# Performance work log

Hardware: AMD Instinct MI355X
Metric: run time of the kernel (lower is better)

The kernel has to match this reference:

```python
import jax, jax.numpy as jnp
import numpy as np

B, L, K, NR, S = 512, 1024, 8, 512, 20  # batch, seq_len, n_matrices, n_rates, alphabet
EXT = 26  # extended alphabet (20 std aa + 6 special), pad of 6 in call()


def _expm(A):
    """Differentiable matrix exponential for small batched matrices (..., n, n).
    Scaling-and-squaring with an order-16 Taylor series (fixed 6 squarings).
    Matches tf.linalg.expm to high accuracy for the small-norm tau*Q here."""
    SQ = 6
    A = A / jnp.asarray(2.0 ** SQ, A.dtype)
    n = A.shape[-1]
    I = jnp.eye(n, dtype=A.dtype)
    P = I + A
    T = A
    for i in range(2, 17):
        T = jnp.matmul(T, A) / i
        P = P + T
    for _ in range(SQ):
        P = jnp.matmul(P, P)
    return P


def setup_inputs() -> dict:
    key = jax.random.key(0)
    k1, k2, k3, k4, k5 = jax.random.split(key, 5)
    return {
        "inputs": jax.random.randint(k1, (B, L), 0, EXT, dtype=jnp.int32),
        "rate_indices": jax.random.randint(k2, (B,), 0, NR, dtype=jnp.int32),
        "tau_kernel": jax.random.normal(k3, (NR,), dtype=jnp.float32),
        "exchangeability_kernel": jax.random.normal(k4, (K, S, S), dtype=jnp.float32),
        "frequencies": jax.random.uniform(k5, (S,), dtype=jnp.float32, minval=0.01, maxval=1.0),
    }


def reference(inputs, rate_indices, tau_kernel, exchangeability_kernel, frequencies):
    b, l = inputs.shape
    mask = inputs < S                                   # (b, L) std-aa mask
    std = jnp.where(mask, inputs, 0)                    # clamp special tokens to 0
    maskf = mask.astype(jnp.float32)[:, :, None, None]  # (b, L, 1, 1)

    # make_R: symmetrize, softplus, zero diagonal
    eye = jnp.eye(S, dtype=jnp.float32)
    R = jax.nn.softplus(0.5 * (exchangeability_kernel + jnp.swapaxes(exchangeability_kernel, -1, -2)))
    R = R * (1.0 - eye)

    # make_rate_matrix: Q = R * pi, subtract row-sum diagonal, normalize by expected rate
    Q = R * frequencies[None, None, :]                  # (k, s, s)
    diag = jnp.sum(Q, axis=-1, keepdims=True)           # (k, s, 1)
    Q = Q - diag * eye
    mue = jnp.sum(frequencies[None, :, None] * diag, axis=-2, keepdims=True)  # (k, 1, 1)
    Q = Q / jnp.maximum(mue, 1e-16)

    # per-sequence evolutionary times
    tau = jax.nn.softplus(tau_kernel)[rate_indices]     # (b,)

    # batched small-matrix expm: (b, k, s, s)
    P = _expm(tau[:, None, None, None] * Q[None])

    # gather ancestral probability rows: (b, L, k, s)
    anc = P[jnp.arange(b)[:, None], :, std, :]
    anc = anc * maskf
    anc = jnp.pad(anc, ((0, 0), (0, 0), (0, 0), (0, EXT - S)))  # pad 20 -> 26
    rest = jax.nn.one_hot(inputs, EXT, dtype=jnp.float32)[:, :, None, :] * (1.0 - maskf)
    anc = anc + rest                                    # (b, L, k, 26)
    return anc.reshape(b, l, -1)                        # (b, L, k*26)
```

## Files before the change

kernel.cpp:

```cpp
#include <hip/hip_runtime.h>
#include <math.h>

#define B    512
#define L    1024
#define K    8
#define NR   512
#define S    20
#define EXT  26
#define SS   (S*S)
#define PD   24
#define PDSQ (PD*PD)
#define ROWF (K*EXT)
#define BROW (L*ROWF)

__device__ __forceinline__ float softplusf(float x) {
    return fmaxf(x, 0.0f) + log1pf(expf(-fabsf(x)));
}

__device__ __forceinline__ void wave_fence() {
    __builtin_amdgcn_wave_barrier();
}

__global__ __launch_bounds__(512, 2) void fused_kernel(
    const int*   __restrict__ inputs,
    const int*   __restrict__ rate_indices,
    const float* __restrict__ tau_kernel,
    const float* __restrict__ exch,
    const float* __restrict__ freq,
    float* __restrict__ out)
{
    __shared__ __align__(16) float M[K][2][PDSQ];
    __shared__ __align__(16) float Row[EXT*ROWF];
    __shared__ int   inp_sh[L];
    __shared__ float diag_sh[K][S];
    __shared__ float mue_sh[K];

    const int b    = blockIdx.x;
    const int t    = threadIdx.x;
    const int w    = t >> 6;
    const int lane = t & 63;
    const int li = lane >> 3, lj = lane & 7;
    const int r0 = 3*li, c0 = 3*lj;

    for (int u = t; u < L; u += 512) inp_sh[u] = inputs[b*L + u];
    for (int e = t; e < EXT*ROWF; e += 512) {
        int row = e / ROWF, c = e - row*ROWF;
        int k = c / EXT, s = c - k*EXT;
        if (row < S) {
            if (s >= S) Row[e] = 0.f;
        } else {
            Row[e] = (s == row) ? 1.f : 0.f;
        }
    }
    float* M0 = &M[w][0][0];
    float* M1 = &M[w][1][0];
    for (int e = lane; e < 2*PDSQ; e += 64) M0[e] = 0.f;
    float tau = softplusf(tau_kernel[rate_indices[b]]);
    wave_fence();

    const float* E = exch + w * SS;
    for (int e = lane; e < SS; e += 64) {
        int r = e / S, c = e - r*S;
        float v = 0.f;
        if (r != c)
            v = softplusf(0.5f * (E[r*S + c] + E[c*S + r])) * freq[c];
        M0[r*PD + c] = v;
    }
    wave_fence();
    if (lane < S) {
        float d = 0.f;
        #pragma unroll
        for (int j = 0; j < S; ++j) d += M0[lane*PD + j];
        diag_sh[w][lane] = d;
    }
    wave_fence();
    if (lane == 0) {
        float m = 0.f;
        #pragma unroll
        for (int s = 0; s < S; ++s) m += freq[s] * diag_sh[w][s];
        mue_sh[w] = fmaxf(m, 1e-16f);
    }
    wave_fence();
    {
        float scale = tau * 0.015625f;
        float mue   = mue_sh[w];
        for (int e = lane; e < SS; e += 64) {
            int r = e / S, c = e - r*S;
            float v = (r == c) ? -diag_sh[w][r] : M0[r*PD + c];
            M0[r*PD + c] = (v / mue) * scale;
        }
    }
    wave_fence();

    float Ac[S][3];
    #pragma unroll
    for (int j = 0; j < S; ++j) {
        #pragma unroll
        for (int d = 0; d < 3; ++d)
            Ac[j][d] = M0[j*PD + c0 + d];
    }

    float P[3][3];
    #pragma unroll
    for (int dr = 0; dr < 3; ++dr)
        #pragma unroll
        for (int dc = 0; dc < 3; ++dc) {
            int r = r0 + dr, c = c0 + dc;
            P[dr][dc] = M0[r*PD + c] + ((r == c && r < S) ? 1.f : 0.f);
        }

    const float* Tc = M0;
    float* Tn = M1;
    #pragma unroll 1
    for (int i = 2; i <= 10; ++i) {
        float C[3][3] = {{0.f,0.f,0.f},{0.f,0.f,0.f},{0.f,0.f,0.f}};
        #pragma unroll
        for (int jc = 0; jc < 5; ++jc) {
            float4 a0 = *(const float4*)&Tc[(r0+0)*PD + 4*jc];
            float4 a1 = *(const float4*)&Tc[(r0+1)*PD + 4*jc];
            float4 a2 = *(const float4*)&Tc[(r0+2)*PD + 4*jc];
            float t0[4] = {a0.x, a0.y, a0.z, a0.w};
            float t1[4] = {a1.x, a1.y, a1.z, a1.w};
            float t2[4] = {a2.x, a2.y, a2.z, a2.w};
            #pragma unroll
            for (int dj = 0; dj < 4; ++dj) {
                int j = 4*jc + dj;
                #pragma unroll
                for (int dc = 0; dc < 3; ++dc) {
                    C[0][dc] = fmaf(t0[dj], Ac[j][dc], C[0][dc]);
                    C[1][dc] = fmaf(t1[dj], Ac[j][dc], C[1][dc]);
                    C[2][dc] = fmaf(t2[dj], Ac[j][dc], C[2][dc]);
                }
            }
        }
        float inv = 1.0f / (float)i;
        #pragma unroll
        for (int dr = 0; dr < 3; ++dr)
            #pragma unroll
            for (int dc = 0; dc < 3; ++dc) {
                C[dr][dc] *= inv;
                P[dr][dc] += C[dr][dc];
                Tn[(r0+dr)*PD + c0 + dc] = C[dr][dc];
            }
        wave_fence();
        float* tmp = (float*)Tc; Tc = Tn; Tn = tmp;
    }

    #pragma unroll 1
    for (int sq = 0; sq < 6; ++sq) {
        #pragma unroll
        for (int dr = 0; dr < 3; ++dr)
            #pragma unroll
            for (int dc = 0; dc < 3; ++dc)
                Tn[(r0+dr)*PD + c0 + dc] = P[dr][dc];
        wave_fence();
        const float* Pb = Tn;
        float C[3][3] = {{0.f,0.f,0.f},{0.f,0.f,0.f},{0.f,0.f,0.f}};
        #pragma unroll
        for (int jc = 0; jc < 5; ++jc) {
            float4 a0 = *(const float4*)&Pb[(r0+0)*PD + 4*jc];
            float4 a1 = *(const float4*)&Pb[(r0+1)*PD + 4*jc];
            float4 a2 = *(const float4*)&Pb[(r0+2)*PD + 4*jc];
            float t0[4] = {a0.x, a0.y, a0.z, a0.w};
            float t1[4] = {a1.x, a1.y, a1.z, a1.w};
            float t2[4] = {a2.x, a2.y, a2.z, a2.w};
            float cb[4][3];
            #pragma unroll
            for (int dj = 0; dj < 4; ++dj)
                #pragma unroll
                for (int dc = 0; dc < 3; ++dc)
                    cb[dj][dc] = Pb[(4*jc + dj)*PD + c0 + dc];
            #pragma unroll
            for (int dj = 0; dj < 4; ++dj)
                #pragma unroll
                for (int dc = 0; dc < 3; ++dc) {
                    C[0][dc] = fmaf(t0[dj], cb[dj][dc], C[0][dc]);
                    C[1][dc] = fmaf(t1[dj], cb[dj][dc], C[1][dc]);
                    C[2][dc] = fmaf(t2[dj], cb[dj][dc], C[2][dc]);
                }
        }
        #pragma unroll
        for (int dr = 0; dr < 3; ++dr)
            #pragma unroll
            for (int dc = 0; dc < 3; ++dc)
                P[dr][dc] = C[dr][dc];
        float* tmp = (float*)Tc; Tc = Tn; Tn = tmp;
        wave_fence();
    }

    #pragma unroll
    for (int dr = 0; dr < 3; ++dr) {
        int r = r0 + dr; if (r >= S) continue;
        #pragma unroll
        for (int dc = 0; dc < 3; ++dc) {
            int c = c0 + dc; if (c >= S) continue;
            Row[r*ROWF + w*EXT + c] = P[dr][dc];
        }
    }
    __syncthreads();

    int l0[13], qq[13];
    {
        int uu = t;
        #pragma unroll
        for (int j = 0; j < 13; ++j) {
            l0[j] = uu / 52;
            qq[j] = uu - l0[j] * 52;
            uu += 512;
        }
    }
    const float4* Row4 = (const float4*)Row;
    float4* out4 = (float4*)out + (size_t)b * (BROW/4);
    #pragma unroll 1
    for (int i = 0; i < 8; ++i) {
        int lbase = i << 7;
        int ubase = t + i * 6656;
        #pragma unroll
        for (int j = 0; j < 13; ++j) {
            int inp = inp_sh[l0[j] + lbase];
            out4[ubase + (j << 9)] = Row4[inp * 52 + qq[j]];
        }
    }
}

extern "C" void kernel_launch(void* const* d_in, const int* in_sizes, int n_in,
                              void* d_out, int out_size, void* d_ws, size_t ws_size,
                              hipStream_t stream) {
    const int*   inputs  = (const int*)  d_in[0];
    const int*   rate_ix = (const int*)  d_in[1];
    const float* tau_k   = (const float*)d_in[2];
    const float* exch    = (const float*)d_in[3];
    const float* freq    = (const float*)d_in[4];
    float* out = (float*)d_out;

    (void)d_ws; (void)ws_size;

    fused_kernel<<<B, 512, 0, stream>>>(inputs, rate_ix, tau_k, exch, freq, out);
}
```

Before: 476.6 us.

## Write special-token rows before expm and store transposed P for squaring

```diff
diff --git a/kernel.cpp b/kernel.cpp
--- a/kernel.cpp
+++ b/kernel.cpp
@@ -21,6 +21,12 @@
     __builtin_amdgcn_wave_barrier();
 }
 
+__device__ __forceinline__ float onehotv(int e, int inp) {
+    int k  = (e * 1261) >> 15;
+    int me = e - 26 * k;
+    return (me == inp) ? 1.f : 0.f;
+}
+
 __global__ __launch_bounds__(512, 2) void fused_kernel(
     const int*   __restrict__ inputs,
     const int*   __restrict__ rate_indices,
@@ -30,7 +36,7 @@
     float* __restrict__ out)
 {
     __shared__ __align__(16) float M[K][2][PDSQ];
-    __shared__ __align__(16) float Row[EXT*ROWF];
+    __shared__ __align__(16) float Row[S*ROWF];
     __shared__ int   inp_sh[L];
     __shared__ float diag_sh[K][S];
     __shared__ float mue_sh[K];
@@ -42,16 +48,49 @@
     const int li = lane >> 3, lj = lane & 7;
     const int r0 = 3*li, c0 = 3*lj;
 
-    for (int u = t; u < L; u += 512) inp_sh[u] = inputs[b*L + u];
-    for (int e = t; e < EXT*ROWF; e += 512) {
-        int row = e / ROWF, c = e - row*ROWF;
-        int k = c / EXT, s = c - k*EXT;
-        if (row < S) {
-            if (s >= S) Row[e] = 0.f;
-        } else {
-            Row[e] = (s == row) ? 1.f : 0.f;
-        }
-    }
+    const int* gin = inputs + b * L;
+    float4* out4 = (float4*)out + (size_t)b * (BROW/4);
+
+    int l0[13], qq[13];
+    {
+        int uu = t;
+        #pragma unroll
+        for (int j = 0; j < 13; ++j) {
+            l0[j] = uu / 52;
+            qq[j] = uu - l0[j] * 52;
+            uu += 512;
+        }
+    }
+
+    for (int u = t; u < L; u += 512) inp_sh[u] = gin[u];
+
+    #pragma unroll 1
+    for (int i = 0; i < 8; ++i) {
+        int lbase = i << 7;
+        int ubase = t + i * 6656;
+        #pragma unroll
+        for (int j = 0; j < 13; ++j) {
+            int inp = gin[l0[j] + lbase];
+            if (inp >= S) {
+                int e = qq[j] << 2;
+                float4 v;
+                v.x = onehotv(e,     inp);
+                v.y = onehotv(e + 1, inp);
+                v.z = onehotv(e + 2, inp);
+                v.w = onehotv(e + 3, inp);
+                out4[ubase + (j << 9)] = v;
+            }
+        }
+    }
+
+    for (int idx = t; idx < S * 48; idx += 512) {
+        int r   = idx / 48;
+        int c48 = idx - r * 48;
+        int k   = c48 / 6;
+        int s   = 20 + (c48 - k * 6);
+        Row[r*ROWF + k*EXT + s] = 0.f;
+    }
+
     float* M0 = &M[w][0][0];
     float* M1 = &M[w][1][0];
     for (int e = lane; e < 2*PDSQ; e += 64) M0[e] = 0.f;
@@ -146,45 +185,46 @@
         float* tmp = (float*)Tc; Tc = Tn; Tn = tmp;
     }
 
+    float* X = M0;
+    float* Y = M1;
     #pragma unroll 1
     for (int sq = 0; sq < 6; ++sq) {
         #pragma unroll
         for (int dr = 0; dr < 3; ++dr)
             #pragma unroll
-            for (int dc = 0; dc < 3; ++dc)
-                Tn[(r0+dr)*PD + c0 + dc] = P[dr][dc];
+            for (int dc = 0; dc < 3; ++dc) {
+                X[(r0+dr)*PD + c0+dc] = P[dr][dc];
+                Y[(c0+dc)*PD + r0+dr] = P[dr][dc];
+            }
         wave_fence();
-        const float* Pb = Tn;
         float C[3][3] = {{0.f,0.f,0.f},{0.f,0.f,0.f},{0.f,0.f,0.f}};
         #pragma unroll
         for (int jc = 0; jc < 5; ++jc) {
-            float4 a0 = *(const float4*)&Pb[(r0+0)*PD + 4*jc];
-            float4 a1 = *(const float4*)&Pb[(r0+1)*PD + 4*jc];
-            float4 a2 = *(const float4*)&Pb[(r0+2)*PD + 4*jc];
-            float t0[4] = {a0.x, a0.y, a0.z, a0.w};
-            float t1[4] = {a1.x, a1.y, a1.z, a1.w};
-            float t2[4] = {a2.x, a2.y, a2.z, a2.w};
-            float cb[4][3];
+            float4 a0 = *(const float4*)&X[(r0+0)*PD + 4*jc];
+            float4 a1 = *(const float4*)&X[(r0+1)*PD + 4*jc];
+            float4 a2 = *(const float4*)&X[(r0+2)*PD + 4*jc];
+            float4 b0 = *(const float4*)&Y[(c0+0)*PD + 4*jc];
+            float4 b1 = *(const float4*)&Y[(c0+1)*PD + 4*jc];
+            float4 b2 = *(const float4*)&Y[(c0+2)*PD + 4*jc];
+            float ta[3][4] = {{a0.x,a0.y,a0.z,a0.w},
+                              {a1.x,a1.y,a1.z,a1.w},
+                              {a2.x,a2.y,a2.z,a2.w}};
+            float tb[3][4] = {{b0.x,b0.y,b0.z,b0.w},
+                              {b1.x,b1.y,b1.z,b1.w},
+                              {b2.x,b2.y,b2.z,b2.w}};
             #pragma unroll
             for (int dj = 0; dj < 4; ++dj)
                 #pragma unroll
-                for (int dc = 0; dc < 3; ++dc)
-                    cb[dj][dc] = Pb[(4*jc + dj)*PD + c0 + dc];
-            #pragma unroll
-            for (int dj = 0; dj < 4; ++dj)
-                #pragma unroll
-                for (int dc = 0; dc < 3; ++dc) {
-                    C[0][dc] = fmaf(t0[dj], cb[dj][dc], C[0][dc]);
-                    C[1][dc] = fmaf(t1[dj], cb[dj][dc], C[1][dc]);
-                    C[2][dc] = fmaf(t2[dj], cb[dj][dc], C[2][dc]);
-                }
+                for (int dr = 0; dr < 3; ++dr)
+                    #pragma unroll
+                    for (int dc = 0; dc < 3; ++dc)
+                        C[dr][dc] = fmaf(ta[dr][dj], tb[dc][dj], C[dr][dc]);
         }
         #pragma unroll
         for (int dr = 0; dr < 3; ++dr)
             #pragma unroll
             for (int dc = 0; dc < 3; ++dc)
                 P[dr][dc] = C[dr][dc];
-        float* tmp = (float*)Tc; Tc = Tn; Tn = tmp;
         wave_fence();
     }
 
@@ -199,18 +239,7 @@
     }
     __syncthreads();
 
-    int l0[13], qq[13];
-    {
-        int uu = t;
-        #pragma unroll
-        for (int j = 0; j < 13; ++j) {
-            l0[j] = uu / 52;
-            qq[j] = uu - l0[j] * 52;
-            uu += 512;
-        }
-    }
     const float4* Row4 = (const float4*)Row;
-    float4* out4 = (float4*)out + (size_t)b * (BROW/4);
     #pragma unroll 1
     for (int i = 0; i < 8; ++i) {
         int lbase = i << 7;
@@ -218,7 +247,8 @@
         #pragma unroll
         for (int j = 0; j < 13; ++j) {
             int inp = inp_sh[l0[j] + lbase];
-            out4[ubase + (j << 9)] = Row4[inp * 52 + qq[j]];
+            if (inp < S)
+                out4[ubase + (j << 9)] = Row4[inp * 52 + qq[j]];
         }
     }
 }
```

Result: slower. 520.2 us (+9.2%).

## Split into expm LUT kernel and a two-block-per-batch store kernel

Applied to the files above, without the earlier changes.

```diff
diff --git a/kernel.cpp b/kernel.cpp
--- a/kernel.cpp
+++ b/kernel.cpp
@@ -12,6 +12,10 @@
 #define PDSQ (PD*PD)
 #define ROWF (K*EXT)
 #define BROW (L*ROWF)
+#define LUTF (EXT*ROWF)
+#define LUT4 (LUTF/4)
+#define B4   (BROW/4)
+#define H4   (B4/2)
 
 __device__ __forceinline__ float softplusf(float x) {
     return fmaxf(x, 0.0f) + log1pf(expf(-fabsf(x)));
@@ -21,8 +25,7 @@
     __builtin_amdgcn_wave_barrier();
 }
 
-__global__ __launch_bounds__(512, 2) void fused_kernel(
-    const int*   __restrict__ inputs,
+__global__ __launch_bounds__(512, 2) void expm_lut_kernel(
     const int*   __restrict__ rate_indices,
     const float* __restrict__ tau_kernel,
     const float* __restrict__ exch,
@@ -30,8 +33,7 @@
     float* __restrict__ out)
 {
     __shared__ __align__(16) float M[K][2][PDSQ];
-    __shared__ __align__(16) float Row[EXT*ROWF];
-    __shared__ int   inp_sh[L];
+    __shared__ __align__(16) float Row[LUTF];
     __shared__ float diag_sh[K][S];
     __shared__ float mue_sh[K];
 
@@ -42,19 +44,20 @@
     const int li = lane >> 3, lj = lane & 7;
     const int r0 = 3*li, c0 = 3*lj;
 
-    for (int u = t; u < L; u += 512) inp_sh[u] = inputs[b*L + u];
-    for (int e = t; e < EXT*ROWF; e += 512) {
+    for (int e = t; e < LUTF; e += 512) {
         int row = e / ROWF, c = e - row*ROWF;
         int k = c / EXT, s = c - k*EXT;
+        (void)k;
         if (row < S) {
             if (s >= S) Row[e] = 0.f;
         } else {
             Row[e] = (s == row) ? 1.f : 0.f;
         }
     }
+
     float* M0 = &M[w][0][0];
     float* M1 = &M[w][1][0];
-    for (int e = lane; e < 2*PDSQ; e += 64) M0[e] = 0.f;
+    for (int e = lane; e < PDSQ; e += 64) M0[e] = 0.f;
     float tau = softplusf(tau_kernel[rate_indices[b]]);
     wave_fence();
 
@@ -112,7 +115,7 @@
     const float* Tc = M0;
     float* Tn = M1;
     #pragma unroll 1
-    for (int i = 2; i <= 10; ++i) {
+    for (int i = 2; i <= 8; ++i) {
         float C[3][3] = {{0.f,0.f,0.f},{0.f,0.f,0.f},{0.f,0.f,0.f}};
         #pragma unroll
         for (int jc = 0; jc < 5; ++jc) {
@@ -184,7 +187,6 @@
             #pragma unroll
             for (int dc = 0; dc < 3; ++dc)
                 P[dr][dc] = C[dr][dc];
-        float* tmp = (float*)Tc; Tc = Tn; Tn = tmp;
         wave_fence();
     }
 
@@ -197,6 +199,32 @@
             Row[r*ROWF + w*EXT + c] = P[dr][dc];
         }
     }
+    __syncthreads();
+
+    const float4* Row4 = (const float4*)Row;
+    float4* out4 = (float4*)out + (size_t)b * B4;
+    for (int u = t; u < LUT4; u += 512) {
+        float4 v = Row4[u];
+        out4[u] = v;
+        out4[H4 + u] = v;
+    }
+}
+
+__global__ __launch_bounds__(512) void store_kernel(
+    const int* __restrict__ inputs,
+    float* __restrict__ out)
+{
+    __shared__ __align__(16) float4 Row4[LUT4];
+    __shared__ int inp_sh[L/2];
+
+    int blk = blockIdx.x;
+    int b = blk >> 1, h = blk & 1;
+    int t = threadIdx.x;
+
+    float4* base4 = (float4*)out + (size_t)b * B4 + (size_t)h * H4;
+
+    for (int u = t; u < LUT4; u += 512) Row4[u] = base4[u];
+    inp_sh[t] = inputs[b * L + h * (L/2) + t];
     __syncthreads();
 
     int l0[13], qq[13];
@@ -209,16 +237,15 @@
             uu += 512;
         }
     }
-    const float4* Row4 = (const float4*)Row;
-    float4* out4 = (float4*)out + (size_t)b * (BROW/4);
+
     #pragma unroll 1
-    for (int i = 0; i < 8; ++i) {
+    for (int i = 0; i < 4; ++i) {
         int lbase = i << 7;
         int ubase = t + i * 6656;
         #pragma unroll
         for (int j = 0; j < 13; ++j) {
             int inp = inp_sh[l0[j] + lbase];
-            out4[ubase + (j << 9)] = Row4[inp * 52 + qq[j]];
+            base4[ubase + (j << 9)] = Row4[inp * 52 + qq[j]];
         }
     }
 }
@@ -235,5 +262,6 @@
 
     (void)d_ws; (void)ws_size;
 
-    fused_kernel<<<B, 512, 0, stream>>>(inputs, rate_ix, tau_k, exch, freq, out);
-}
+    expm_lut_kernel<<<B, 512, 0, stream>>>(rate_ix, tau_k, exch, freq, out);
+    store_kernel<<<B * 2, 512, 0, stream>>>(inputs, out);
+}
```

New measurement: 487.3 us. 1.02x slower.
